# Kernel optimization log

Hardware: AMD Instinct MI355X
Metric: run time of the kernel (lower is better)

## Reference

```python
import jax, jax.numpy as jnp
import numpy as np

N_HEAD = 16

def setup_inputs() -> dict:
    key = jax.random.key(0)
    ks = jax.random.split(key, 5)
    d = 1024
    x = jax.random.normal(ks[0], (2, 2048, d), dtype=jnp.float32)
    Wqkv = jax.random.normal(ks[1], (d, 3 * d), dtype=jnp.float32) * (1.0 / np.sqrt(d))
    bqkv = jnp.zeros((3 * d,), dtype=jnp.float32)
    Wproj = jax.random.normal(ks[2], (d, d), dtype=jnp.float32) * (1.0 / np.sqrt(d))
    bproj = jnp.zeros((d,), dtype=jnp.float32)
    return {"x": x, "Wqkv": Wqkv, "bqkv": bqkv, "Wproj": Wproj, "bproj": bproj}


def reference(x, Wqkv, bqkv, Wproj, bproj):
    B, T, C = x.shape
    H = N_HEAD
    Dh = C // H
    qkv = x @ Wqkv + bqkv                      # [B, T, 3C]
    q, k, v = jnp.split(qkv, 3, axis=-1)
    # [B, T, C] -> [B, H, T, Dh]
    q = q.reshape(B, T, H, Dh).transpose(0, 2, 1, 3)
    k = k.reshape(B, T, H, Dh).transpose(0, 2, 1, 3)
    v = v.reshape(B, T, H, Dh).transpose(0, 2, 1, 3)
    scale = 1.0 / np.sqrt(Dh)
    att = jnp.einsum('bhqd,bhkd->bhqk', q, k) * scale
    causal = jnp.tril(jnp.ones((T, T), dtype=bool))
    att = jnp.where(causal[None, None, :, :], att, jnp.float32(-jnp.inf))
    att = jax.nn.softmax(att, axis=-1)
    y = jnp.einsum('bhqk,bhkd->bhqd', att, v)  # [B, H, T, Dh]
    y = y.transpose(0, 2, 1, 3).reshape(B, T, C)
    return y @ Wproj + bproj
```

## Files before the change

kernel.cpp:

```cpp
#include <hip/hip_runtime.h>
#include <math.h>


typedef __attribute__((ext_vector_type(8))) short short8;
typedef __attribute__((ext_vector_type(4))) short short4v;
typedef __attribute__((ext_vector_type(4))) float floatx4;

__device__ __forceinline__ unsigned short f2bf(float f) {
  unsigned u = __float_as_uint(f);
  return (unsigned short)((u + 0x7fff + ((u >> 16) & 1)) >> 16);
}

__device__ __forceinline__ void gld16(const unsigned short* g, unsigned short* l) {
  __builtin_amdgcn_global_load_lds(
      (const __attribute__((address_space(1))) unsigned int*)g,
      (__attribute__((address_space(3))) unsigned int*)l, 16, 0, 0);
}

__device__ __forceinline__ void pack_a_body(const float* __restrict__ in,
                                            unsigned short* __restrict__ out,
                                            int K, int m0, int k0,
                                            unsigned short (*lds)[72], int t) {
  {
    int ml = t >> 2, kl = (t & 3) * 16;
    const float4* p = (const float4*)(in + (size_t)(m0 + ml) * K + k0 + kl);
    unsigned short* q = &lds[ml][kl];
#pragma unroll
    for (int c = 0; c < 4; ++c) {
      float4 v = p[c];
      q[c * 4 + 0] = f2bf(v.x);
      q[c * 4 + 1] = f2bf(v.y);
      q[c * 4 + 2] = f2bf(v.z);
      q[c * 4 + 3] = f2bf(v.w);
    }
  }
  __syncthreads();
  int chunk = t >> 3, sub = t & 7;
  int mt = chunk >> 3, kc = chunk & 7;
  unsigned short tmp[16];
#pragma unroll
  for (int j2 = 0; j2 < 2; ++j2)
#pragma unroll
    for (int j = 0; j < 8; ++j)
      tmp[j2 * 8 + j] = lds[mt * 16 + sub * 2 + j2][kc * 8 + j];
  size_t ofs = ((size_t)(m0 >> 4) + mt) * (16 * (size_t)K) +
               ((size_t)(k0 >> 3) + kc) * 128 + sub * 16;
  *(int4*)(out + ofs) = *(int4*)(tmp);
  *(int4*)(out + ofs + 8) = *(int4*)(tmp + 8);
}

__device__ __forceinline__ void pack_bt_body(const float* __restrict__ in,
                                             unsigned short* __restrict__ out,
                                             int K, int N, int n0, int k0,
                                             unsigned short (*lds)[72], int t) {
  {
    int kl = t >> 2, nl = (t & 3) * 16;
    const float4* p = (const float4*)(in + (size_t)(k0 + kl) * N + n0 + nl);
#pragma unroll
    for (int c = 0; c < 4; ++c) {
      float4 v = p[c];
      lds[nl + c * 4 + 0][kl] = f2bf(v.x);
      lds[nl + c * 4 + 1][kl] = f2bf(v.y);
      lds[nl + c * 4 + 2][kl] = f2bf(v.z);
      lds[nl + c * 4 + 3][kl] = f2bf(v.w);
    }
  }
  __syncthreads();
  int chunk = t >> 3, sub = t & 7;
  int nt = chunk >> 3, kc = chunk & 7;
  unsigned short tmp[16];
#pragma unroll
  for (int j2 = 0; j2 < 2; ++j2)
#pragma unroll
    for (int j = 0; j < 8; ++j)
      tmp[j2 * 8 + j] = lds[nt * 16 + sub * 2 + j2][kc * 8 + j];
  size_t ofs = ((size_t)(n0 >> 4) + nt) * (16 * (size_t)K) +
               ((size_t)(k0 >> 3) + kc) * 128 + sub * 16;
  *(int4*)(out + ofs) = *(int4*)(tmp);
  *(int4*)(out + ofs + 8) = *(int4*)(tmp + 8);
}

__global__ __launch_bounds__(256) void pack_all(
    const float* __restrict__ x, const float* __restrict__ Wqkv,
    const float* __restrict__ Wproj, unsigned short* __restrict__ xbf,
    unsigned short* __restrict__ wqkvF, unsigned short* __restrict__ wprojF) {
  __shared__ __align__(16) unsigned short lds[64][72];
  const int b = blockIdx.x, t = threadIdx.x;
  if (b < 1024) {
    pack_a_body(x, xbf, 1024, (b >> 4) * 64, (b & 15) * 64, lds, t);
  } else if (b < 1792) {
    int b2 = b - 1024;
    pack_bt_body(Wqkv, wqkvF, 1024, 3072, (b2 % 48) * 64, (b2 / 48) * 64, lds, t);
  } else {
    int b3 = b - 1792;
    pack_bt_body(Wproj, wprojF, 1024, 1024, (b3 & 15) * 64, (b3 >> 4) * 64, lds, t);
  }
}

template <int MODE>
__global__ __launch_bounds__(256, 3) void gemm_lds(
    const unsigned short* __restrict__ A, const unsigned short* __restrict__ B,
    const float* __restrict__ bias, float* __restrict__ Cout,
    unsigned short* __restrict__ Qb, unsigned short* __restrict__ Kb,
    unsigned short* __restrict__ Vt, int M, int N, int K) {
  const int tid = threadIdx.x;
  const int wave = tid >> 6, lane = tid & 63;
  const int quad = lane >> 4, l15 = lane & 15;
  const int wr = wave >> 1, wc = wave & 1;

  const int nbn = N >> 7;
  const int colsPerX = nbn >> 3;
  const int xcd = (int)(blockIdx.x & 7);
  const int idx = (int)(blockIdx.x >> 3);
  const int bn = xcd * colsPerX + (colsPerX == 1 ? 0 : (idx % colsPerX));
  const int bm = (colsPerX == 1) ? idx : (idx / colsPerX);

  const int mt0 = bm * 8;
  const int nt0 = bn * 8;

  __shared__ __align__(16) unsigned short As[8192];
  __shared__ __align__(16) unsigned short Bs[8192];

  const unsigned short* spA[4];
  const unsigned short* spB[4];
#pragma unroll
  for (int j = 0; j < 4; ++j) {
    int c = wave * 4 + j;
    spA[j] = A + ((size_t)(mt0 + (c >> 1))) * (16 * (size_t)K) +
             (c & 1) * 512 + lane * 8;
    spB[j] = B + ((size_t)(nt0 + (c >> 1))) * (16 * (size_t)K) +
             (c & 1) * 512 + lane * 8;
  }

  floatx4 acc[4][4];
#pragma unroll
  for (int i = 0; i < 4; ++i)
#pragma unroll
    for (int j = 0; j < 4; ++j) acc[i][j] = (floatx4)0.0f;

  const int fofs = quad * 128 + l15 * 8;
  const int nk = K >> 6;

  for (int kk = 0; kk < nk; ++kk) {
#pragma unroll
    for (int j = 0; j < 4; ++j) {
      gld16(spA[j], &As[(wave * 4 + j) * 512]);
      gld16(spB[j], &Bs[(wave * 4 + j) * 512]);
      spA[j] += 1024;
      spB[j] += 1024;
    }
    __syncthreads();

#pragma unroll
    for (int ks = 0; ks < 2; ++ks) {
      short8 fa[4], fb[4];
#pragma unroll
      for (int im = 0; im < 4; ++im)
        fa[im] = *(const short8*)&As[((wr * 4 + im) * 2 + ks) * 512 + fofs];
#pragma unroll
      for (int in = 0; in < 4; ++in)
        fb[in] = *(const short8*)&Bs[((wc * 4 + in) * 2 + ks) * 512 + fofs];
#pragma unroll
      for (int im = 0; im < 4; ++im)
#pragma unroll
        for (int in = 0; in < 4; ++in)
          acc[im][in] = __builtin_amdgcn_mfma_f32_16x16x32_bf16(
              fa[im], fb[in], acc[im][in], 0, 0, 0);
    }
    if (kk + 1 < nk) __syncthreads();
  }

  const int m0w = bm * 128 + wr * 64;
  const int n0w = bn * 128 + wc * 64;

  if (MODE == 0) {
    const float QSCALE = 0.18033688f;
#pragma unroll
    for (int im = 0; im < 4; ++im) {
      int mbase = m0w + im * 16 + quad * 4;
      int bb = mbase >> 11, tb = mbase & 2047;
#pragma unroll
      for (int in = 0; in < 4; ++in) {
        int n = n0w + in * 16 + l15;
        float bv = bias[n];
        int which = n >> 10;
        int h = (n >> 6) & 15;
        int d = n & 63;
        size_t bh_ = (size_t)(bb * 16 + h);
        if (which == 2) {
          size_t base = bh_ * 131072 + (size_t)(d >> 4) * 32768 +
                        (size_t)(tb >> 3) * 128 + (d & 15) * 8 + (tb & 7);
          short4v pk;
#pragma unroll
          for (int r = 0; r < 4; ++r) pk[r] = (short)f2bf(acc[im][in][r] + bv);
          *(short4v*)(Vt + base) = pk;
        } else {
          size_t base = bh_ * 131072 + (size_t)(tb >> 4) * 1024 +
                        (d >> 3) * 128 + (tb & 15) * 8 + (d & 7);
          if (which == 0) {
#pragma unroll
            for (int r = 0; r < 4; ++r)
              Qb[base + r * 8] = f2bf((acc[im][in][r] + bv) * QSCALE);
          } else {
#pragma unroll
            for (int r = 0; r < 4; ++r)
              Kb[base + r * 8] = f2bf(acc[im][in][r] + bv);
          }
        }
      }
    }
  } else {
#pragma unroll
    for (int im = 0; im < 4; ++im) {
      int mbase = m0w + im * 16 + quad * 4;
#pragma unroll
      for (int in = 0; in < 4; ++in) {
        int n = n0w + in * 16 + l15;
        float bv = bias[n];
#pragma unroll
        for (int r = 0; r < 4; ++r)
          Cout[(size_t)(mbase + r) * N + n] = acc[im][in][r] + bv;
      }
    }
  }
}

__global__ __launch_bounds__(256) void attn_mfma(
    const unsigned short* __restrict__ Q, const unsigned short* __restrict__ K,
    const unsigned short* __restrict__ Vt, unsigned short* __restrict__ Y) {
  const int bh = blockIdx.x;
  const int wave = threadIdx.x >> 6;
  const int lane = threadIdx.x & 63;
  const int s = ((int)(gridDim.y - 1 - blockIdx.y)) * 4 + wave;
  const int quad = lane >> 4, l15 = lane & 15;

  __shared__ __align__(16) unsigned short Plds[4][16][72];
  unsigned short(*P)[72] = Plds[wave];

  const int t0 = s * 16;
  const unsigned short* Qb = Q + (size_t)bh * 131072;
  const unsigned short* Kb = K + (size_t)bh * 131072;
  const unsigned short* Vb = Vt + (size_t)bh * 131072;
  const int lofs = quad * 128 + l15 * 8;

  short8 qf[2];
#pragma unroll
  for (int c = 0; c < 2; ++c)
    qf[c] = *(const short8*)(Qb + (size_t)s * 1024 + c * 512 + lofs);

  floatx4 o[4];
#pragma unroll
  for (int in = 0; in < 4; ++in) o[in] = (floatx4)0.0f;
  float l_acc = 0.f;

  const int ntiles = (s >> 2) + 1;

  short8 kf[4][2], vf[4][2];
#pragma unroll
  for (int in = 0; in < 4; ++in) {
    const unsigned short* kp = Kb + (size_t)in * 1024 + lofs;
    kf[in][0] = *(const short8*)(kp);
    kf[in][1] = *(const short8*)(kp + 512);
  }

  for (int jt = 0; jt < ntiles; ++jt) {
    const int kt0 = jt * 64;
#pragma unroll
    for (int in = 0; in < 4; ++in) {
      const unsigned short* vp =
          Vb + (size_t)in * 32768 + (size_t)jt * 1024 + lofs;
      vf[in][0] = *(const short8*)(vp);
      vf[in][1] = *(const short8*)(vp + 512);
    }

    floatx4 sa[4];
#pragma unroll
    for (int in = 0; in < 4; ++in) {
      floatx4 z = (floatx4)0.0f;
      z = __builtin_amdgcn_mfma_f32_16x16x32_bf16(kf[in][0], qf[0], z, 0, 0, 0);
      sa[in] = __builtin_amdgcn_mfma_f32_16x16x32_bf16(kf[in][1], qf[1], z, 0, 0, 0);
    }

    if (jt + 1 < ntiles) {
#pragma unroll
      for (int in = 0; in < 4; ++in) {
        const unsigned short* kp = Kb + (size_t)(jt * 4 + 4 + in) * 1024 + lofs;
        kf[in][0] = *(const short8*)(kp);
        kf[in][1] = *(const short8*)(kp + 512);
      }
    }

    if (jt == ntiles - 1) {
#pragma unroll
      for (int in = 0; in < 4; ++in) {
        int keyb = kt0 + in * 16 + quad * 4;
#pragma unroll
        for (int r = 0; r < 4; ++r)
          if (keyb + r > t0 + l15) sa[in][r] = -__builtin_inff();
      }
    }

#pragma unroll
    for (int in = 0; in < 4; ++in)
#pragma unroll
      for (int r = 0; r < 4; ++r) {
        float p = exp2f(sa[in][r]);
        sa[in][r] = p;
        l_acc += p;
      }

#pragma unroll
    for (int in = 0; in < 4; ++in) {
      uint2 pk;
      pk.x = (__float_as_uint(sa[in][0]) >> 16) |
             (__float_as_uint(sa[in][1]) & 0xFFFF0000u);
      pk.y = (__float_as_uint(sa[in][2]) >> 16) |
             (__float_as_uint(sa[in][3]) & 0xFFFF0000u);
      *(uint2*)&P[l15][in * 16 + quad * 4] = pk;
    }
    short8 pf0 = *(const short8*)&P[l15][quad * 8];
    short8 pf1 = *(const short8*)&P[l15][32 + quad * 8];

#pragma unroll
    for (int in = 0; in < 4; ++in) {
      o[in] = __builtin_amdgcn_mfma_f32_16x16x32_bf16(pf0, vf[in][0], o[in], 0, 0, 0);
      o[in] = __builtin_amdgcn_mfma_f32_16x16x32_bf16(pf1, vf[in][1], o[in], 0, 0, 0);
    }
  }

  l_acc += __shfl_xor(l_acc, 16);
  l_acc += __shfl_xor(l_acc, 32);

  const int b_ = bh >> 4, h = bh & 15;
  float inv[4];
#pragma unroll
  for (int r = 0; r < 4; ++r)
    inv[r] = 1.f / __shfl(l_acc, (lane & 48) | (quad * 4 + r));

  size_t mt = (size_t)(b_ * 128 + s);
#pragma unroll
  for (int in = 0; in < 4; ++in) {
    size_t cbase = (size_t)(h * 8 + in * 2 + (l15 >> 3)) * 128 + (l15 & 7);
#pragma unroll
    for (int r = 0; r < 4; ++r)
      Y[mt * 16384 + cbase + (quad * 4 + r) * 8] = f2bf(o[in][r] * inv[r]);
  }
}

extern "C" void kernel_launch(void* const* d_in, const int* in_sizes, int n_in,
                              void* d_out, int out_size, void* d_ws,
                              size_t ws_size, hipStream_t stream) {
  const float* x = (const float*)d_in[0];
  const float* Wqkv = (const float*)d_in[1];
  const float* bqkv = (const float*)d_in[2];
  const float* Wproj = (const float*)d_in[3];
  const float* bproj = (const float*)d_in[4];
  float* out = (float*)d_out;

  const int C = 1024;
  const int M = 4096;

  char* ws = (char*)d_ws;
  unsigned short* qbuf = (unsigned short*)ws;
  unsigned short* kbuf = (unsigned short*)(ws + 8388608);
  unsigned short* vtbuf = (unsigned short*)(ws + 16777216);
  unsigned short* ybuf = (unsigned short*)(ws + 25165824);
  unsigned short* xbf = (unsigned short*)(ws + 33554432);
  unsigned short* wqkvF = (unsigned short*)(ws + 41943040);
  unsigned short* wprojF = (unsigned short*)(ws + 48234496);

  dim3 blk(256);
  pack_all<<<dim3(2048), blk, 0, stream>>>(x, Wqkv, Wproj, xbf, wqkvF, wprojF);
  gemm_lds<0><<<dim3((M / 128) * (3 * C / 128)), blk, 0, stream>>>(
      xbf, wqkvF, bqkv, nullptr, qbuf, kbuf, vtbuf, M, 3 * C, C);
  attn_mfma<<<dim3(32, 32), blk, 0, stream>>>(qbuf, kbuf, vtbuf, ybuf);
  gemm_lds<1><<<dim3((M / 128) * (C / 128)), blk, 0, stream>>>(
      ybuf, wprojF, bproj, out, nullptr, nullptr, nullptr, M, C, C);
}
```

Measured before the change: 180.9 us.

## Switch attention to 32x32 MFMA tiles with permlane-based P repacking

Rewrites the attention kernel so each wave handles 32 query rows using 32x32x16 bf16 MFMAs instead of 16x16x32, and changes the Q/K/Vt layouts written by the QKV GEMM epilogue to match. The LDS round-trip for P is replaced by v_cvt_pk_bf16_f32 plus permlane32_swap register shuffles. The grid is flattened to 1D and mapped so heads are grouped per XCD, with heavier causal tiles scheduled first, and launch bounds request two blocks per CU. This aims to cut LDS traffic, K/V reload per query row and instruction count, at the cost of higher register pressure and a changed rounding path for P.

```diff
diff --git a/kernel.cpp b/kernel.cpp
--- a/kernel.cpp
+++ b/kernel.cpp
@@ -5,10 +5,25 @@
 typedef __attribute__((ext_vector_type(8))) short short8;
 typedef __attribute__((ext_vector_type(4))) short short4v;
 typedef __attribute__((ext_vector_type(4))) float floatx4;
+typedef __attribute__((ext_vector_type(16))) float floatx16;
+typedef __attribute__((ext_vector_type(2))) unsigned int uint2v;
+typedef __attribute__((ext_vector_type(4))) unsigned int uint4v;
 
 __device__ __forceinline__ unsigned short f2bf(float f) {
   unsigned u = __float_as_uint(f);
   return (unsigned short)((u + 0x7fff + ((u >> 16) & 1)) >> 16);
+}
+
+__device__ __forceinline__ unsigned cvtpk(float a, float b) {
+  unsigned r;
+  asm("v_cvt_pk_bf16_f32 %0, %1, %2" : "=v"(r) : "v"(a), "v"(b));
+  return r;
+}
+
+__device__ __forceinline__ short8 mk8(unsigned w0, unsigned w1, unsigned w2,
+                                      unsigned w3) {
+  uint4v v = {w0, w1, w2, w3};
+  return __builtin_bit_cast(short8, v);
 }
 
 __device__ __forceinline__ void gld16(const unsigned short* g, unsigned short* l) {
@@ -188,15 +203,19 @@
         int d = n & 63;
         size_t bh_ = (size_t)(bb * 16 + h);
         if (which == 2) {
-          size_t base = bh_ * 131072 + (size_t)(d >> 4) * 32768 +
-                        (size_t)(tb >> 3) * 128 + (d & 15) * 8 + (tb & 7);
+          size_t base = bh_ * 131072 + (size_t)(d >> 5) * 65536 +
+                        (size_t)(tb >> 4) * 512 +
+                        (size_t)((d & 31) + 32 * ((tb & 15) >> 3)) * 8 +
+                        (tb & 7);
           short4v pk;
 #pragma unroll
           for (int r = 0; r < 4; ++r) pk[r] = (short)f2bf(acc[im][in][r] + bv);
           *(short4v*)(Vt + base) = pk;
         } else {
-          size_t base = bh_ * 131072 + (size_t)(tb >> 4) * 1024 +
-                        (d >> 3) * 128 + (tb & 15) * 8 + (d & 7);
+          size_t base = bh_ * 131072 + (size_t)(tb >> 5) * 2048 +
+                        (size_t)(d >> 4) * 512 +
+                        (size_t)((tb & 31) + 32 * ((d & 15) >> 3)) * 8 +
+                        (d & 7);
           if (which == 0) {
 #pragma unroll
             for (int r = 0; r < 4; ++r)
@@ -225,125 +244,134 @@
   }
 }
 
-__global__ __launch_bounds__(256) void attn_mfma(
+__device__ __forceinline__ void pack_swap(const floatx16& s, short8& lo,
+                                          short8& hi) {
+  unsigned P0 = cvtpk(s[0], s[1]), P1 = cvtpk(s[2], s[3]);
+  unsigned P2 = cvtpk(s[4], s[5]), P3 = cvtpk(s[6], s[7]);
+  unsigned P4 = cvtpk(s[8], s[9]), P5 = cvtpk(s[10], s[11]);
+  unsigned P6 = cvtpk(s[12], s[13]), P7 = cvtpk(s[14], s[15]);
+  uint2v a = __builtin_amdgcn_permlane32_swap(P0, P2, false, false);
+  uint2v b = __builtin_amdgcn_permlane32_swap(P1, P3, false, false);
+  uint2v c = __builtin_amdgcn_permlane32_swap(P4, P6, false, false);
+  uint2v d = __builtin_amdgcn_permlane32_swap(P5, P7, false, false);
+  lo = mk8(a.x, b.x, a.y, b.y);
+  hi = mk8(c.x, d.x, c.y, d.y);
+}
+
+__global__ __launch_bounds__(256, 2) void attn_mfma(
     const unsigned short* __restrict__ Q, const unsigned short* __restrict__ K,
     const unsigned short* __restrict__ Vt, unsigned short* __restrict__ Y) {
-  const int bh = blockIdx.x;
+  const int b = (int)blockIdx.x;
+  const int xcd = b & 7, qi = b >> 3;
+  const int bh = xcd * 4 + (qi & 3);
+  const int m = 15 - (qi >> 2);
   const int wave = threadIdx.x >> 6;
   const int lane = threadIdx.x & 63;
-  const int s = ((int)(gridDim.y - 1 - blockIdx.y)) * 4 + wave;
-  const int quad = lane >> 4, l15 = lane & 15;
-
-  __shared__ __align__(16) unsigned short Plds[4][16][72];
-  unsigned short(*P)[72] = Plds[wave];
-
-  const int t0 = s * 16;
+  const int j = m * 4 + wave;
+  const int t0 = j * 32;
+  const int l31 = lane & 31, h = lane >> 5;
+
   const unsigned short* Qb = Q + (size_t)bh * 131072;
   const unsigned short* Kb = K + (size_t)bh * 131072;
   const unsigned short* Vb = Vt + (size_t)bh * 131072;
-  const int lofs = quad * 128 + l15 * 8;
-
-  short8 qf[2];
-#pragma unroll
-  for (int c = 0; c < 2; ++c)
-    qf[c] = *(const short8*)(Qb + (size_t)s * 1024 + c * 512 + lofs);
-
-  floatx4 o[4];
-#pragma unroll
-  for (int in = 0; in < 4; ++in) o[in] = (floatx4)0.0f;
-  float l_acc = 0.f;
-
-  const int ntiles = (s >> 2) + 1;
-
-  short8 kf[4][2], vf[4][2];
-#pragma unroll
-  for (int in = 0; in < 4; ++in) {
-    const unsigned short* kp = Kb + (size_t)in * 1024 + lofs;
-    kf[in][0] = *(const short8*)(kp);
-    kf[in][1] = *(const short8*)(kp + 512);
+  const int lofs = lane * 8;
+
+  short8 qf[4];
+#pragma unroll
+  for (int c = 0; c < 4; ++c)
+    qf[c] = *(const short8*)(Qb + (size_t)j * 2048 + c * 512 + lofs);
+
+  floatx16 o0 = (floatx16)0.0f, o1 = (floatx16)0.0f;
+  float lp[4] = {0.f, 0.f, 0.f, 0.f};
+
+  const int ntiles = (j >> 1) + 1;
+
+  short8 kf[2][4];
+#pragma unroll
+  for (int c = 0; c < 4; ++c) {
+    kf[0][c] = *(const short8*)(Kb + c * 512 + lofs);
+    kf[1][c] = *(const short8*)(Kb + 2048 + c * 512 + lofs);
   }
 
   for (int jt = 0; jt < ntiles; ++jt) {
-    const int kt0 = jt * 64;
-#pragma unroll
-    for (int in = 0; in < 4; ++in) {
-      const unsigned short* vp =
-          Vb + (size_t)in * 32768 + (size_t)jt * 1024 + lofs;
-      vf[in][0] = *(const short8*)(vp);
-      vf[in][1] = *(const short8*)(vp + 512);
-    }
-
-    floatx4 sa[4];
-#pragma unroll
-    for (int in = 0; in < 4; ++in) {
-      floatx4 z = (floatx4)0.0f;
-      z = __builtin_amdgcn_mfma_f32_16x16x32_bf16(kf[in][0], qf[0], z, 0, 0, 0);
-      sa[in] = __builtin_amdgcn_mfma_f32_16x16x32_bf16(kf[in][1], qf[1], z, 0, 0, 0);
+    short8 vf[2][4];
+#pragma unroll
+    for (int kc = 0; kc < 4; ++kc) {
+      vf[0][kc] = *(const short8*)(Vb + (size_t)(4 * jt + kc) * 512 + lofs);
+      vf[1][kc] =
+          *(const short8*)(Vb + 65536 + (size_t)(4 * jt + kc) * 512 + lofs);
+    }
+
+    floatx16 sa0 = (floatx16)0.0f, sa1 = (floatx16)0.0f;
+#pragma unroll
+    for (int c = 0; c < 4; ++c) {
+      sa0 = __builtin_amdgcn_mfma_f32_32x32x16_bf16(kf[0][c], qf[c], sa0, 0, 0, 0);
+      sa1 = __builtin_amdgcn_mfma_f32_32x32x16_bf16(kf[1][c], qf[c], sa1, 0, 0, 0);
     }
 
     if (jt + 1 < ntiles) {
 #pragma unroll
-      for (int in = 0; in < 4; ++in) {
-        const unsigned short* kp = Kb + (size_t)(jt * 4 + 4 + in) * 1024 + lofs;
-        kf[in][0] = *(const short8*)(kp);
-        kf[in][1] = *(const short8*)(kp + 512);
+      for (int c = 0; c < 4; ++c) {
+        kf[0][c] =
+            *(const short8*)(Kb + (size_t)(2 * jt + 2) * 2048 + c * 512 + lofs);
+        kf[1][c] =
+            *(const short8*)(Kb + (size_t)(2 * jt + 3) * 2048 + c * 512 + lofs);
       }
     }
 
     if (jt == ntiles - 1) {
 #pragma unroll
-      for (int in = 0; in < 4; ++in) {
-        int keyb = kt0 + in * 16 + quad * 4;
-#pragma unroll
-        for (int r = 0; r < 4; ++r)
-          if (keyb + r > t0 + l15) sa[in][r] = -__builtin_inff();
+      for (int r = 0; r < 16; ++r) {
+        int row = (r & 3) + 8 * (r >> 2) + 4 * h;
+        int key = jt * 64 + row;
+        if (key > t0 + l31) sa0[r] = -__builtin_inff();
+        if (key + 32 > t0 + l31) sa1[r] = -__builtin_inff();
       }
     }
 
 #pragma unroll
-    for (int in = 0; in < 4; ++in)
-#pragma unroll
-      for (int r = 0; r < 4; ++r) {
-        float p = exp2f(sa[in][r]);
-        sa[in][r] = p;
-        l_acc += p;
-      }
-
-#pragma unroll
-    for (int in = 0; in < 4; ++in) {
-      uint2 pk;
-      pk.x = (__float_as_uint(sa[in][0]) >> 16) |
-             (__float_as_uint(sa[in][1]) & 0xFFFF0000u);
-      pk.y = (__float_as_uint(sa[in][2]) >> 16) |
-             (__float_as_uint(sa[in][3]) & 0xFFFF0000u);
-      *(uint2*)&P[l15][in * 16 + quad * 4] = pk;
-    }
-    short8 pf0 = *(const short8*)&P[l15][quad * 8];
-    short8 pf1 = *(const short8*)&P[l15][32 + quad * 8];
-
-#pragma unroll
-    for (int in = 0; in < 4; ++in) {
-      o[in] = __builtin_amdgcn_mfma_f32_16x16x32_bf16(pf0, vf[in][0], o[in], 0, 0, 0);
-      o[in] = __builtin_amdgcn_mfma_f32_16x16x32_bf16(pf1, vf[in][1], o[in], 0, 0, 0);
-    }
-  }
-
-  l_acc += __shfl_xor(l_acc, 16);
+    for (int r = 0; r < 16; ++r) {
+      float p0 = exp2f(sa0[r]);
+      float p1 = exp2f(sa1[r]);
+      sa0[r] = p0;
+      sa1[r] = p1;
+      lp[r & 3] += p0 + p1;
+    }
+
+    short8 pb0, pb1, pb2, pb3;
+    pack_swap(sa0, pb0, pb1);
+    pack_swap(sa1, pb2, pb3);
+
+    o0 = __builtin_amdgcn_mfma_f32_32x32x16_bf16(vf[0][0], pb0, o0, 0, 0, 0);
+    o1 = __builtin_amdgcn_mfma_f32_32x32x16_bf16(vf[1][0], pb0, o1, 0, 0, 0);
+    o0 = __builtin_amdgcn_mfma_f32_32x32x16_bf16(vf[0][1], pb1, o0, 0, 0, 0);
+    o1 = __builtin_amdgcn_mfma_f32_32x32x16_bf16(vf[1][1], pb1, o1, 0, 0, 0);
+    o0 = __builtin_amdgcn_mfma_f32_32x32x16_bf16(vf[0][2], pb2, o0, 0, 0, 0);
+    o1 = __builtin_amdgcn_mfma_f32_32x32x16_bf16(vf[1][2], pb2, o1, 0, 0, 0);
+    o0 = __builtin_amdgcn_mfma_f32_32x32x16_bf16(vf[0][3], pb3, o0, 0, 0, 0);
+    o1 = __builtin_amdgcn_mfma_f32_32x32x16_bf16(vf[1][3], pb3, o1, 0, 0, 0);
+  }
+
+  float l_acc = (lp[0] + lp[1]) + (lp[2] + lp[3]);
   l_acc += __shfl_xor(l_acc, 32);
-
-  const int b_ = bh >> 4, h = bh & 15;
-  float inv[4];
-#pragma unroll
-  for (int r = 0; r < 4; ++r)
-    inv[r] = 1.f / __shfl(l_acc, (lane & 48) | (quad * 4 + r));
-
-  size_t mt = (size_t)(b_ * 128 + s);
-#pragma unroll
-  for (int in = 0; in < 4; ++in) {
-    size_t cbase = (size_t)(h * 8 + in * 2 + (l15 >> 3)) * 128 + (l15 & 7);
-#pragma unroll
-    for (int r = 0; r < 4; ++r)
-      Y[mt * 16384 + cbase + (quad * 4 + r) * 8] = f2bf(o[in][r] * inv[r]);
+  const float inv = 1.0f / l_acc;
+
+  const int b_ = bh >> 4, hh = bh & 15;
+  const int mglob = b_ * 2048 + t0 + l31;
+  const size_t mofs = (size_t)(mglob >> 4) * 16384 + (size_t)(mglob & 15) * 8;
+#pragma unroll
+  for (int db = 0; db < 2; ++db) {
+    const floatx16& o = db ? o1 : o0;
+#pragma unroll
+    for (int g = 0; g < 4; ++g) {
+      int d0 = db * 32 + 8 * g + 4 * h;
+      int kf0 = hh * 64 + d0;
+      size_t ofs = mofs + (size_t)(kf0 >> 3) * 128 + (kf0 & 7);
+      short4v pk;
+#pragma unroll
+      for (int r = 0; r < 4; ++r) pk[r] = (short)f2bf(o[4 * g + r] * inv);
+      *(short4v*)(Y + ofs) = pk;
+    }
   }
 }
 
@@ -373,7 +401,7 @@
   pack_all<<<dim3(2048), blk, 0, stream>>>(x, Wqkv, Wproj, xbf, wqkvF, wprojF);
   gemm_lds<0><<<dim3((M / 128) * (3 * C / 128)), blk, 0, stream>>>(
       xbf, wqkvF, bqkv, nullptr, qbuf, kbuf, vtbuf, M, 3 * C, C);
-  attn_mfma<<<dim3(32, 32), blk, 0, stream>>>(qbuf, kbuf, vtbuf, ybuf);
+  attn_mfma<<<dim3(512), blk, 0, stream>>>(qbuf, kbuf, vtbuf, ybuf);
   gemm_lds<1><<<dim3((M / 128) * (C / 128)), blk, 0, stream>>>(
       ybuf, wprojF, bproj, out, nullptr, nullptr, nullptr, M, C, C);
 }
```

After: 179.5 us. Within noise of the previous version (-0.8%).
